# Performance work log

Measured on AMD Instinct MI355X. Metric: run time of the kernel, lower is better.

Reference implementation:

```python
import jax, jax.numpy as jnp
import numpy as np

N_HEADS = 16
NEG_INF = -1e9


def setup_inputs() -> dict:
    key = jax.random.key(0)
    ks = jax.random.split(key, 6)
    B, S, D = 2, 2048, 1024
    scale = 0.02
    return {
        "x": jax.random.normal(ks[0], (B, S, D), dtype=jnp.float32),
        "padding_mask": jnp.ones((B, S), dtype=jnp.float32),
        "wq_w": jax.random.normal(ks[1], (D, D), dtype=jnp.float32) * scale,
        "wq_b": jnp.zeros((D,), dtype=jnp.float32),
        "wk_w": jax.random.normal(ks[2], (D, D), dtype=jnp.float32) * scale,
        "wk_b": jnp.zeros((D,), dtype=jnp.float32),
        "wv_w": jax.random.normal(ks[3], (D, D), dtype=jnp.float32) * scale,
        "wv_b": jnp.zeros((D,), dtype=jnp.float32),
        "wo_w": jax.random.normal(ks[4], (D, D), dtype=jnp.float32) * scale,
        "wo_b": jnp.zeros((D,), dtype=jnp.float32),
    }


def _split_heads(t, B, S, H, depth):
    # (B, S, D) -> (B, H, S, depth)
    return t.reshape(B, S, H, depth).transpose(0, 2, 1, 3)


def reference(x, padding_mask, wq_w, wq_b, wk_w, wk_b, wv_w, wv_b, wo_w, wo_b):
    B, S, D = x.shape
    H = N_HEADS
    depth = D // H

    q = _split_heads(x @ wq_w + wq_b, B, S, H, depth)
    k = _split_heads(x @ wk_w + wk_b, B, S, H, depth)
    v = _split_heads(x @ wv_w + wv_b, B, S, H, depth)

    scale = jnp.sqrt(jnp.asarray(depth, dtype=jnp.float32))
    logits = jnp.einsum('bhqd,bhkd->bhqk', q, k) / scale  # (B,H,S,S)

    causal = jnp.tril(jnp.ones((S, S), dtype=jnp.float32))  # lower-triangular keep mask
    logits = logits + (1.0 - causal)[None, None] * NEG_INF
    # padding mask: (B, S) -> (B, 1, 1, S), 1 = keep
    logits = logits + (1.0 - padding_mask)[:, None, None, :] * NEG_INF

    attn = jax.nn.softmax(logits, axis=-1)
    # dropout: identity at inference (training=False)
    out = jnp.einsum('bhqk,bhkd->bhqd', attn, v)
    out = out.transpose(0, 2, 1, 3).reshape(B, S, D)
    return out @ wo_w + wo_b
```

## Files before the change

kernel.cpp:

```cpp
#include <hip/hip_runtime.h>
#include <math.h>

#define S_LEN 2048
#define DMODEL 1024
#define NH 16
#define DEPTH 64
#define BATCH 2
#define MTOT (BATCH * S_LEN)

typedef __attribute__((ext_vector_type(8))) short short8;
typedef __attribute__((ext_vector_type(4))) short short4v;
typedef __attribute__((ext_vector_type(4))) float floatx4;

typedef const __attribute__((address_space(1))) unsigned gas_u32;
typedef __attribute__((address_space(3))) unsigned las_u32;

__device__ __forceinline__ short f2bf(float f) {
    union { float f; unsigned u; } v; v.f = f;
    unsigned r = v.u + 0x7fffu + ((v.u >> 16) & 1u);
    return (short)(r >> 16);
}

__device__ __forceinline__ unsigned packbf2(float lo, float hi) {
    union { float f; unsigned u; } a, b;
    a.f = lo; b.f = hi;
    return __builtin_amdgcn_perm(b.u + 0x8000u, a.u + 0x8000u, 0x07060302u);
}

__device__ __forceinline__ floatx4 mfma16(short8 a, short8 b, floatx4 c) {
    return __builtin_amdgcn_mfma_f32_16x16x32_bf16(a, b, c, 0, 0, 0);
}

#if __has_builtin(__builtin_amdgcn_mfma_f32_16x16x16bf16_1k)
__device__ __forceinline__ floatx4 mfma16k16(short4v a, short4v b, floatx4 c) {
    return __builtin_amdgcn_mfma_f32_16x16x16bf16_1k(a, b, c, 0, 0, 0);
}
#else
__device__ __forceinline__ floatx4 mfma16k16(short4v a, short4v b, floatx4 c) {
    asm volatile("v_mfma_f32_16x16x16_bf16 %0, %1, %2, %0\n\ts_nop 7\n\ts_nop 7"
                 : "+v"(c) : "v"(a), "v"(b));
    return c;
}
#endif

__global__ __launch_bounds__(256) void prep_kernel(const float* __restrict__ x,
                                                   short* __restrict__ xb,
                                                   const float* __restrict__ w0, const float* __restrict__ w1,
                                                   const float* __restrict__ w2, const float* __restrict__ w3,
                                                   short* __restrict__ o0, short* __restrict__ o1,
                                                   short* __restrict__ o2, short* __restrict__ o3) {
    const int bid = blockIdx.x;
    const int tid = threadIdx.x;
    if (bid < 4096) {
        int i = (bid * 256 + tid) * 4;
        float4 v = *(const float4*)(x + i);
        short4v o;
        o.x = f2bf(v.x); o.y = f2bf(v.y); o.z = f2bf(v.z); o.w = f2bf(v.w);
        *(short4v*)(xb + i) = o;
        return;
    }
    const int b2 = bid - 4096;
    const int z = b2 >> 10;
    const int rem = b2 & 1023;
    const int bx = rem & 31, by = rem >> 5;
    const float* src; short* dst;
    switch (z) {
        case 0: src = w0; dst = o0; break;
        case 1: src = w1; dst = o1; break;
        case 2: src = w2; dst = o2; break;
        default: src = w3; dst = o3; break;
    }
    __shared__ float tile[32][33];
    const int tx = tid & 31, ty = tid >> 5;
    int c = bx * 32 + tx;
    int r0 = by * 32;
#pragma unroll
    for (int i = 0; i < 4; i++)
        tile[ty + i * 8][tx] = src[(size_t)(r0 + ty + i * 8) * DMODEL + c];
    __syncthreads();
    int co = by * 32 + tx;
    int ro = bx * 32;
#pragma unroll
    for (int i = 0; i < 4; i++)
        dst[(size_t)(ro + ty + i * 8) * DMODEL + co] = f2bf(tile[tx][ty + i * 8]);
}

__device__ __forceinline__ void stage_tile(const short* __restrict__ src, int row0, int k0,
                                           short* dstLds, int tid) {
#pragma unroll
    for (int s = 0; s < 4; s++) {
        const int p = s * 4096 + tid * 16;
        const int q = p ^ (((p >> 7) & 7) << 4);
        const char* srcp = (const char*)src + (size_t)(row0 + (q >> 7)) * (DMODEL * 2)
                         + k0 * 2 + (q & 127);
        __builtin_amdgcn_global_load_lds((gas_u32*)srcp,
                                         (las_u32*)((char*)dstLds + p), 16, 0, 0);
    }
}

__device__ __forceinline__ void gemm_core(const short* __restrict__ A,
                                          const short* __restrict__ Bt,
                                          int m0, int n0,
                                          short* Ab0, short* Ab1, short* Bb0, short* Bb1,
                                          floatx4 acc[4][4]) {
    const int tid = threadIdx.x;
    const int lane = tid & 63;
    const int w = tid >> 6;
    const int wr = w >> 1, wc = w & 1;
    const int l15 = lane & 15, lhi = lane >> 4;
    const int swz = (l15 & 7) << 4;

    stage_tile(A, m0, 0, Ab0, tid);
    stage_tile(Bt, n0, 0, Bb0, tid);
    asm volatile("s_waitcnt vmcnt(0)" ::: "memory");
    __syncthreads();

    for (int ks = 0; ks < 16; ks++) {
        const char* Ac = (const char*)((ks & 1) ? Ab1 : Ab0);
        const char* Bc = (const char*)((ks & 1) ? Bb1 : Bb0);
        if (ks < 15) {
            stage_tile(A, m0, (ks + 1) * 64, (ks & 1) ? Ab0 : Ab1, tid);
            stage_tile(Bt, n0, (ks + 1) * 64, (ks & 1) ? Bb0 : Bb1, tid);
        }
#pragma unroll
        for (int kkb = 0; kkb < 128; kkb += 64) {
            short8 af[4], bf[4];
#pragma unroll
            for (int i = 0; i < 4; i++) {
                int row = wr * 64 + i * 16 + l15;
                af[i] = *(const short8*)(Ac + ((row * 128 + kkb + lhi * 16) ^ swz));
            }
#pragma unroll
            for (int j = 0; j < 4; j++) {
                int row = wc * 64 + j * 16 + l15;
                bf[j] = *(const short8*)(Bc + ((row * 128 + kkb + lhi * 16) ^ swz));
            }
#pragma unroll
            for (int i = 0; i < 4; i++)
#pragma unroll
                for (int j = 0; j < 4; j++)
                    acc[i][j] = mfma16(af[i], bf[j], acc[i][j]);
        }
        asm volatile("s_waitcnt vmcnt(0)" ::: "memory");
        __syncthreads();
    }
}

__global__ __launch_bounds__(256) void gemm_qkv(const short* __restrict__ A,
                                                const short* __restrict__ wq, const short* __restrict__ wk,
                                                const short* __restrict__ wv,
                                                const float* __restrict__ bq, const float* __restrict__ bk,
                                                const float* __restrict__ bv,
                                                short* __restrict__ qh, short* __restrict__ kh,
                                                short* __restrict__ vt) {
    __shared__ __align__(16) short Ab[2][8192];
    __shared__ __align__(16) short Bb[2][8192];
    const int bid = blockIdx.x;
    const int xcd = bid & 7;
    const int slot = bid >> 3;
    const int msub = slot & 3;
    const int c = slot >> 2;
    const int nt = c & 7;
    const int mode = c >> 3;
    const int m0 = (xcd * 4 + msub) * 128;
    const int n0 = nt * 128;

    const short* Bt = (mode == 0) ? wq : (mode == 1) ? wk : wv;
    const float* bias = (mode == 0) ? bq : (mode == 1) ? bk : bv;

    floatx4 acc[4][4];
    floatx4 z = {0.f, 0.f, 0.f, 0.f};
#pragma unroll
    for (int i = 0; i < 4; i++)
#pragma unroll
        for (int j = 0; j < 4; j++) acc[i][j] = z;

    gemm_core(A, Bt, m0, n0, Ab[0], Ab[1], Bb[0], Bb[1], acc);

    const int lane = threadIdx.x & 63;
    const int w = threadIdx.x >> 6;
    const int wr = w >> 1, wc = w & 1;
    const int l15 = lane & 15, lhi = lane >> 4;
    const float qscale = (mode == 0) ? 0.125f : 1.0f;
#pragma unroll
    for (int i = 0; i < 4; i++) {
#pragma unroll
        for (int j = 0; j < 4; j++) {
            int n = n0 + wc * 64 + j * 16 + l15;
            float bv_ = bias[n];
            int h = n >> 6, d = n & 63;
            int mbase = m0 + wr * 64 + i * 16 + (lhi << 2);
#pragma unroll
            for (int r = 0; r < 4; r++) {
                int m = mbase + r;
                int b = m >> 11, s = m & 2047;
                short val = f2bf((acc[i][j][r] + bv_) * qscale);
                if (mode == 0)
                    qh[((size_t)(b * NH + h) * S_LEN + s) * DEPTH + d] = val;
                else if (mode == 1)
                    kh[((size_t)(b * NH + h) * S_LEN + s) * DEPTH + d] = val;
                else
                    vt[((size_t)(b * NH + h) * DEPTH + d) * S_LEN + s] = val;
            }
        }
    }
}

__global__ __launch_bounds__(256) void gemm_out(const short* __restrict__ A,
                                                const short* __restrict__ Bt,
                                                const float* __restrict__ bias,
                                                float* __restrict__ out) {
    __shared__ __align__(16) short Ab[2][8192];
    __shared__ __align__(16) short Bb[2][8192];
    const int bid = blockIdx.x;
    const int xcd = bid & 7;
    const int slot = bid >> 3;
    const int msub = slot & 3;
    const int nt = slot >> 2;
    const int m0 = (xcd * 4 + msub) * 128;
    const int n0 = nt * 128;

    floatx4 acc[4][4];
    floatx4 z = {0.f, 0.f, 0.f, 0.f};
#pragma unroll
    for (int i = 0; i < 4; i++)
#pragma unroll
        for (int j = 0; j < 4; j++) acc[i][j] = z;

    gemm_core(A, Bt, m0, n0, Ab[0], Ab[1], Bb[0], Bb[1], acc);

    const int lane = threadIdx.x & 63;
    const int w = threadIdx.x >> 6;
    const int wr = w >> 1, wc = w & 1;
    const int l15 = lane & 15, lhi = lane >> 4;
#pragma unroll
    for (int i = 0; i < 4; i++) {
#pragma unroll
        for (int j = 0; j < 4; j++) {
            int n = n0 + wc * 64 + j * 16 + l15;
            float bv_ = bias[n];
            int mbase = m0 + wr * 64 + i * 16 + (lhi << 2);
#pragma unroll
            for (int r = 0; r < 4; r++) {
                int m = mbase + r;
                out[(size_t)m * DMODEL + n] = acc[i][j][r] + bv_;
            }
        }
    }
}

__constant__ int YCHUNK[16] = {15, 13, 11, 9, 7, 5, 3, 1, 0, 2, 4, 6, 8, 10, 12, 14};

__device__ __forceinline__ void stage_kv(const short* __restrict__ kb_j0,
                                         const short* __restrict__ vb, int j0,
                                         short* kt, short* vt_, int wid, int lane) {
#pragma unroll
    for (int s = 0; s < 2; s++) {
        const int seg = (s * 4 + wid) * 1024;
        const int p = seg + lane * 16;
        const int q = p ^ (((p >> 7) & 7) << 4);
        __builtin_amdgcn_global_load_lds((gas_u32*)((const char*)kb_j0 + q),
                                         (las_u32*)((char*)kt + seg), 16, 0, 0);
        const char* vsrc = (const char*)vb + (size_t)(q >> 7) * (S_LEN * 2) + j0 * 2 + (q & 127);
        __builtin_amdgcn_global_load_lds((gas_u32*)vsrc,
                                         (las_u32*)((char*)vt_ + seg), 16, 0, 0);
    }
}

__global__ __launch_bounds__(256, 2) void attn_kernel(const short* __restrict__ qh,
                                                      const short* __restrict__ kh,
                                                      const short* __restrict__ vt,
                                                      const float* __restrict__ pm,
                                                      short* __restrict__ ao) {
    __shared__ short kbuf[2][4096];
    __shared__ short vbuf[2][4096];
    const int lane = threadIdx.x & 63;
    const int wid = threadIdx.x >> 6;
    const int bh = blockIdx.x;
    const int chunk = YCHUNK[blockIdx.y];
    const int b = bh >> 4, h = bh & 15;
    const short* qbp = qh + (size_t)bh * S_LEN * DEPTH;
    const short* kb = kh + (size_t)bh * S_LEN * DEPTH;
    const short* vb = vt + (size_t)bh * DEPTH * S_LEN;
    const float* pmb = pm + b * S_LEN;
    const int l15 = lane & 15, lhi = lane >> 4;
    const int swz = (l15 & 7) << 4;

    const int qwb = chunk * 128 + wid * 32;

    short8 qf[2][2];
#pragma unroll
    for (int qg = 0; qg < 2; qg++)
#pragma unroll
        for (int c = 0; c < 2; c++)
            qf[qg][c] = *(const short8*)(qbp + (size_t)(qwb + qg * 16 + l15) * DEPTH + c * 32 + lhi * 8);

    float m_r[2] = {-1e30f, -1e30f};
    float l_part[2] = {0.f, 0.f};
    floatx4 oacc[2][4];
    floatx4 z = {0.f, 0.f, 0.f, 0.f};
#pragma unroll
    for (int qg = 0; qg < 2; qg++)
#pragma unroll
        for (int dt = 0; dt < 4; dt++) oacc[qg][dt] = z;

    const int NT = 2 * chunk + 2;
    stage_kv(kb, vb, 0, kbuf[0], vbuf[0], wid, lane);
    __syncthreads();

    for (int t = 0; t < NT; t++) {
        const int cur = t & 1;
        if (t + 1 < NT)
            stage_kv(kb + (size_t)(t + 1) * 64 * DEPTH, vb, (t + 1) * 64,
                     kbuf[cur ^ 1], vbuf[cur ^ 1], wid, lane);
        const int j0 = t * 64;
        if (j0 <= qwb + 31) {
            const short* kt = kbuf[cur];
            const short* vtile = vbuf[cur];
            short8 kf[4][2];
#pragma unroll
            for (int tt = 0; tt < 4; tt++)
#pragma unroll
                for (int c = 0; c < 2; c++) {
                    int off = (((tt * 16 + l15) * 128) + c * 64 + lhi * 16) ^ swz;
                    kf[tt][c] = *(const short8*)((const char*)kt + off);
                }
            floatx4 sacc[2][4];
#pragma unroll
            for (int qg = 0; qg < 2; qg++)
#pragma unroll
                for (int tt = 0; tt < 4; tt++) sacc[qg][tt] = z;
#pragma unroll
            for (int tt = 0; tt < 4; tt++)
#pragma unroll
                for (int c = 0; c < 2; c++) {
                    sacc[0][tt] = mfma16(kf[tt][c], qf[0][c], sacc[0][tt]);
                    sacc[1][tt] = mfma16(kf[tt][c], qf[1][c], sacc[1][tt]);
                }
            short4v vf[4][4];
#pragma unroll
            for (int tt = 0; tt < 4; tt++)
#pragma unroll
                for (int dt = 0; dt < 4; dt++) {
                    int off = (((dt * 16 + l15) * 128) + tt * 32 + lhi * 8) ^ swz;
                    vf[tt][dt] = *(const short4v*)((const char*)vtile + off);
                }
            float pd[16];
#pragma unroll
            for (int tt = 0; tt < 4; tt++) {
                float4 pmv = *(const float4*)(pmb + j0 + tt * 16 + lhi * 4);
                pd[tt * 4 + 0] = (1.f - pmv.x) * -1e9f;
                pd[tt * 4 + 1] = (1.f - pmv.y) * -1e9f;
                pd[tt * 4 + 2] = (1.f - pmv.z) * -1e9f;
                pd[tt * 4 + 3] = (1.f - pmv.w) * -1e9f;
            }
#pragma unroll
            for (int qg = 0; qg < 2; qg++) {
                const int q = qwb + qg * 16 + l15;
                const bool domask = (j0 + 63 > qwb + qg * 16);
                float mx = -1e30f;
#pragma unroll
                for (int tt = 0; tt < 4; tt++)
#pragma unroll
                    for (int r = 0; r < 4; r++) {
                        float v = sacc[qg][tt][r] + pd[tt * 4 + r];
                        if (domask) {
                            int key = j0 + tt * 16 + lhi * 4 + r;
                            v = (key > q) ? -1e30f : v;
                        }
                        sacc[qg][tt][r] = v;
                        mx = fmaxf(mx, v);
                    }
                if (!__all(mx <= m_r[qg] + 12.0f)) {
                    mx = fmaxf(mx, __shfl_xor(mx, 16, 64));
                    mx = fmaxf(mx, __shfl_xor(mx, 32, 64));
                    float mnew = fmaxf(m_r[qg], mx);
                    float sf = __expf(m_r[qg] - mnew);
                    m_r[qg] = mnew;
                    l_part[qg] *= sf;
#pragma unroll
                    for (int r = 0; r < 4; r++) {
                        float sfr = __shfl(sf, lhi * 4 + r, 64);
#pragma unroll
                        for (int dt = 0; dt < 4; dt++) oacc[qg][dt][r] *= sfr;
                    }
                }
#pragma unroll
                for (int tt = 0; tt < 4; tt++) {
                    float p0 = __expf(sacc[qg][tt][0] - m_r[qg]);
                    float p1 = __expf(sacc[qg][tt][1] - m_r[qg]);
                    float p2 = __expf(sacc[qg][tt][2] - m_r[qg]);
                    float p3 = __expf(sacc[qg][tt][3] - m_r[qg]);
                    l_part[qg] += (p0 + p1) + (p2 + p3);
                    union { unsigned u[2]; short4v s; } cv;
                    cv.u[0] = packbf2(p0, p1);
                    cv.u[1] = packbf2(p2, p3);
#pragma unroll
                    for (int dt = 0; dt < 4; dt++)
                        oacc[qg][dt] = mfma16k16(cv.s, vf[tt][dt], oacc[qg][dt]);
                }
            }
        }
        asm volatile("s_waitcnt vmcnt(0)" ::: "memory");
        __syncthreads();
    }

#pragma unroll
    for (int qg = 0; qg < 2; qg++) {
        float lsum = l_part[qg];
        lsum += __shfl_xor(lsum, 16, 64);
        lsum += __shfl_xor(lsum, 32, 64);
        float rinv[4];
#pragma unroll
        for (int r = 0; r < 4; r++)
            rinv[r] = 1.0f / __shfl(lsum, lhi * 4 + r, 64);
#pragma unroll
        for (int dt = 0; dt < 4; dt++) {
            int d = dt * 16 + l15;
#pragma unroll
            for (int r = 0; r < 4; r++) {
                int row = qwb + qg * 16 + lhi * 4 + r;
                float o = oacc[qg][dt][r] * rinv[r];
                ao[((size_t)(b * S_LEN) + row) * DMODEL + h * DEPTH + d] = f2bf(o);
            }
        }
    }
}

extern "C" void kernel_launch(void* const* d_in, const int* in_sizes, int n_in,
                              void* d_out, int out_size, void* d_ws, size_t ws_size,
                              hipStream_t stream) {
    const float* x    = (const float*)d_in[0];
    const float* pm   = (const float*)d_in[1];
    const float* wq_w = (const float*)d_in[2];
    const float* wq_b = (const float*)d_in[3];
    const float* wk_w = (const float*)d_in[4];
    const float* wk_b = (const float*)d_in[5];
    const float* wv_w = (const float*)d_in[6];
    const float* wv_b = (const float*)d_in[7];
    const float* wo_w = (const float*)d_in[8];
    const float* wo_b = (const float*)d_in[9];
    float* out = (float*)d_out;

    char* ws = (char*)d_ws;
    const size_t MB = 1024 * 1024;
    short* xb  = (short*)(ws);
    short* wqb = (short*)(ws + 8 * MB);
    short* wkb = (short*)(ws + 10 * MB);
    short* wvb = (short*)(ws + 12 * MB);
    short* wob = (short*)(ws + 14 * MB);
    short* qh  = (short*)(ws + 16 * MB);
    short* kh  = (short*)(ws + 24 * MB);
    short* vt  = (short*)(ws + 32 * MB);
    short* ao  = (short*)(ws + 40 * MB);

    prep_kernel<<<8192, 256, 0, stream>>>(x, xb, wq_w, wk_w, wv_w, wo_w,
                                          wqb, wkb, wvb, wob);
    gemm_qkv<<<768, 256, 0, stream>>>(xb, wqb, wkb, wvb, wq_b, wk_b, wv_b,
                                      qh, kh, vt);
    attn_kernel<<<dim3(32, 16), 256, 0, stream>>>(qh, kh, vt, pm, ao);
    gemm_out<<<256, 256, 0, stream>>>(ao, wob, wo_b, out);
}
```

Baseline: 129.8 us.

## Use triple-buffered 32-wide K stages with partial vmcnt waits in GEMM core

```diff
diff --git a/kernel.cpp b/kernel.cpp
--- a/kernel.cpp
+++ b/kernel.cpp
@@ -85,14 +85,14 @@
         dst[(size_t)(ro + ty + i * 8) * DMODEL + co] = f2bf(tile[tx][ty + i * 8]);
 }
 
-__device__ __forceinline__ void stage_tile(const short* __restrict__ src, int row0, int k0,
-                                           short* dstLds, int tid) {
-#pragma unroll
-    for (int s = 0; s < 4; s++) {
+__device__ __forceinline__ void stage32(const short* __restrict__ src, int row0, int k0,
+                                        short* dstLds, int tid) {
+#pragma unroll
+    for (int s = 0; s < 2; s++) {
         const int p = s * 4096 + tid * 16;
-        const int q = p ^ (((p >> 7) & 7) << 4);
-        const char* srcp = (const char*)src + (size_t)(row0 + (q >> 7)) * (DMODEL * 2)
-                         + k0 * 2 + (q & 127);
+        const int q = p ^ (((p >> 7) & 3) << 4);
+        const char* srcp = (const char*)src + (size_t)(row0 + (q >> 6)) * (DMODEL * 2)
+                         + k0 * 2 + (q & 63);
         __builtin_amdgcn_global_load_lds((gas_u32*)srcp,
                                          (las_u32*)((char*)dstLds + p), 16, 0, 0);
     }
@@ -101,48 +101,51 @@
 __device__ __forceinline__ void gemm_core(const short* __restrict__ A,
                                           const short* __restrict__ Bt,
                                           int m0, int n0,
-                                          short* Ab0, short* Ab1, short* Bb0, short* Bb1,
+                                          short* Ab, short* Bb,
                                           floatx4 acc[4][4]) {
     const int tid = threadIdx.x;
     const int lane = tid & 63;
     const int w = tid >> 6;
     const int wr = w >> 1, wc = w & 1;
     const int l15 = lane & 15, lhi = lane >> 4;
-    const int swz = (l15 & 7) << 4;
-
-    stage_tile(A, m0, 0, Ab0, tid);
-    stage_tile(Bt, n0, 0, Bb0, tid);
-    asm volatile("s_waitcnt vmcnt(0)" ::: "memory");
-    __syncthreads();
-
-    for (int ks = 0; ks < 16; ks++) {
-        const char* Ac = (const char*)((ks & 1) ? Ab1 : Ab0);
-        const char* Bc = (const char*)((ks & 1) ? Bb1 : Bb0);
-        if (ks < 15) {
-            stage_tile(A, m0, (ks + 1) * 64, (ks & 1) ? Ab0 : Ab1, tid);
-            stage_tile(Bt, n0, (ks + 1) * 64, (ks & 1) ? Bb0 : Bb1, tid);
-        }
-#pragma unroll
-        for (int kkb = 0; kkb < 128; kkb += 64) {
-            short8 af[4], bf[4];
-#pragma unroll
-            for (int i = 0; i < 4; i++) {
-                int row = wr * 64 + i * 16 + l15;
-                af[i] = *(const short8*)(Ac + ((row * 128 + kkb + lhi * 16) ^ swz));
-            }
-#pragma unroll
-            for (int j = 0; j < 4; j++) {
-                int row = wc * 64 + j * 16 + l15;
-                bf[j] = *(const short8*)(Bc + ((row * 128 + kkb + lhi * 16) ^ swz));
-            }
-#pragma unroll
-            for (int i = 0; i < 4; i++)
-#pragma unroll
-                for (int j = 0; j < 4; j++)
-                    acc[i][j] = mfma16(af[i], bf[j], acc[i][j]);
-        }
-        asm volatile("s_waitcnt vmcnt(0)" ::: "memory");
-        __syncthreads();
+
+    int aoff[4], boff[4];
+#pragma unroll
+    for (int i = 0; i < 4; i++) {
+        int arow = wr * 64 + i * 16 + l15;
+        aoff[i] = (arow * 64 + lhi * 16) ^ (((arow >> 1) & 3) << 4);
+        int brow = wc * 64 + i * 16 + l15;
+        boff[i] = (brow * 64 + lhi * 16) ^ (((brow >> 1) & 3) << 4);
+    }
+
+    stage32(A, m0, 0, Ab, tid);
+    stage32(Bt, n0, 0, Bb, tid);
+    stage32(A, m0, 32, Ab + 4096, tid);
+    stage32(Bt, n0, 32, Bb + 4096, tid);
+
+    for (int ks = 0; ks < 32; ks++) {
+        if (ks < 30) {
+            asm volatile("s_waitcnt vmcnt(4)" ::: "memory");
+        } else {
+            asm volatile("s_waitcnt vmcnt(0)" ::: "memory");
+        }
+        asm volatile("s_barrier" ::: "memory");
+        if (ks + 2 < 32) {
+            stage32(A, m0, (ks + 2) * 32, Ab + ((ks + 2) % 3) * 4096, tid);
+            stage32(Bt, n0, (ks + 2) * 32, Bb + ((ks + 2) % 3) * 4096, tid);
+        }
+        const char* Ac = (const char*)(Ab + (ks % 3) * 4096);
+        const char* Bc = (const char*)(Bb + (ks % 3) * 4096);
+        short8 af[4], bf[4];
+#pragma unroll
+        for (int i = 0; i < 4; i++) af[i] = *(const short8*)(Ac + aoff[i]);
+#pragma unroll
+        for (int j = 0; j < 4; j++) bf[j] = *(const short8*)(Bc + boff[j]);
+#pragma unroll
+        for (int i = 0; i < 4; i++)
+#pragma unroll
+            for (int j = 0; j < 4; j++)
+                acc[i][j] = mfma16(af[i], bf[j], acc[i][j]);
     }
 }
 
@@ -153,8 +156,8 @@
                                                 const float* __restrict__ bv,
                                                 short* __restrict__ qh, short* __restrict__ kh,
                                                 short* __restrict__ vt) {
-    __shared__ __align__(16) short Ab[2][8192];
-    __shared__ __align__(16) short Bb[2][8192];
+    __shared__ __align__(16) short Ab[3 * 4096];
+    __shared__ __align__(16) short Bb[3 * 4096];
     const int bid = blockIdx.x;
     const int xcd = bid & 7;
     const int slot = bid >> 3;
@@ -175,7 +178,7 @@
 #pragma unroll
         for (int j = 0; j < 4; j++) acc[i][j] = z;
 
-    gemm_core(A, Bt, m0, n0, Ab[0], Ab[1], Bb[0], Bb[1], acc);
+    gemm_core(A, Bt, m0, n0, Ab, Bb, acc);
 
     const int lane = threadIdx.x & 63;
     const int w = threadIdx.x >> 6;
@@ -210,8 +213,8 @@
                                                 const short* __restrict__ Bt,
                                                 const float* __restrict__ bias,
                                                 float* __restrict__ out) {
-    __shared__ __align__(16) short Ab[2][8192];
-    __shared__ __align__(16) short Bb[2][8192];
+    __shared__ __align__(16) short Ab[3 * 4096];
+    __shared__ __align__(16) short Bb[3 * 4096];
     const int bid = blockIdx.x;
     const int xcd = bid & 7;
     const int slot = bid >> 3;
@@ -227,7 +230,7 @@
 #pragma unroll
         for (int j = 0; j < 4; j++) acc[i][j] = z;
 
-    gemm_core(A, Bt, m0, n0, Ab[0], Ab[1], Bb[0], Bb[1], acc);
+    gemm_core(A, Bt, m0, n0, Ab, Bb, acc);
 
     const int lane = threadIdx.x & 63;
     const int w = threadIdx.x >> 6;
```

Measured after the change: 148.8 us. 14.7% more time.

## Load GEMM B operand directly into registers, drop B LDS staging, add MFMA priority

Applied to the files above, without the earlier changes.

```diff
diff --git a/kernel.cpp b/kernel.cpp
--- a/kernel.cpp
+++ b/kernel.cpp
@@ -98,10 +98,33 @@
     }
 }
 
+__device__ __forceinline__ void loadB(const short* __restrict__ bbase, int ks, short8 bf[8]) {
+#pragma unroll
+    for (int j = 0; j < 4; j++)
+#pragma unroll
+        for (int kk = 0; kk < 2; kk++)
+            bf[j * 2 + kk] = *(const short8*)(bbase + (size_t)(j * 16) * DMODEL + ks * 64 + kk * 32);
+}
+
+__device__ __forceinline__ void mfma_step(const char* Ac, const int aoffs[4][2],
+                                          const short8 bf[8], floatx4 acc[4][4]) {
+#pragma unroll
+    for (int kk = 0; kk < 2; kk++) {
+        short8 af[4];
+#pragma unroll
+        for (int i = 0; i < 4; i++) af[i] = *(const short8*)(Ac + aoffs[i][kk]);
+#pragma unroll
+        for (int i = 0; i < 4; i++)
+#pragma unroll
+            for (int j = 0; j < 4; j++)
+                acc[i][j] = mfma16(af[i], bf[j * 2 + kk], acc[i][j]);
+    }
+}
+
 __device__ __forceinline__ void gemm_core(const short* __restrict__ A,
                                           const short* __restrict__ Bt,
                                           int m0, int n0,
-                                          short* Ab0, short* Ab1, short* Bb0, short* Bb1,
+                                          short* Ab0, short* Ab1,
                                           floatx4 acc[4][4]) {
     const int tid = threadIdx.x;
     const int lane = tid & 63;
@@ -110,51 +133,48 @@
     const int l15 = lane & 15, lhi = lane >> 4;
     const int swz = (l15 & 7) << 4;
 
+    int aoffs[4][2];
+#pragma unroll
+    for (int i = 0; i < 4; i++) {
+        int row = wr * 64 + i * 16 + l15;
+#pragma unroll
+        for (int kk = 0; kk < 2; kk++)
+            aoffs[i][kk] = ((row * 128) + kk * 64 + lhi * 16) ^ swz;
+    }
+    const short* bbase = Bt + (size_t)(n0 + wc * 64 + l15) * DMODEL + lhi * 8;
+
+    short8 b0[8], b1[8];
     stage_tile(A, m0, 0, Ab0, tid);
-    stage_tile(Bt, n0, 0, Bb0, tid);
+    loadB(bbase, 0, b0);
     asm volatile("s_waitcnt vmcnt(0)" ::: "memory");
     __syncthreads();
 
-    for (int ks = 0; ks < 16; ks++) {
-        const char* Ac = (const char*)((ks & 1) ? Ab1 : Ab0);
-        const char* Bc = (const char*)((ks & 1) ? Bb1 : Bb0);
-        if (ks < 15) {
-            stage_tile(A, m0, (ks + 1) * 64, (ks & 1) ? Ab0 : Ab1, tid);
-            stage_tile(Bt, n0, (ks + 1) * 64, (ks & 1) ? Bb0 : Bb1, tid);
-        }
-#pragma unroll
-        for (int kkb = 0; kkb < 128; kkb += 64) {
-            short8 af[4], bf[4];
-#pragma unroll
-            for (int i = 0; i < 4; i++) {
-                int row = wr * 64 + i * 16 + l15;
-                af[i] = *(const short8*)(Ac + ((row * 128 + kkb + lhi * 16) ^ swz));
-            }
-#pragma unroll
-            for (int j = 0; j < 4; j++) {
-                int row = wc * 64 + j * 16 + l15;
-                bf[j] = *(const short8*)(Bc + ((row * 128 + kkb + lhi * 16) ^ swz));
-            }
-#pragma unroll
-            for (int i = 0; i < 4; i++)
-#pragma unroll
-                for (int j = 0; j < 4; j++)
-                    acc[i][j] = mfma16(af[i], bf[j], acc[i][j]);
-        }
+    for (int ks = 0; ks < 16; ks += 2) {
+        if (ks + 1 < 16) {
+            stage_tile(A, m0, (ks + 1) * 64, Ab1, tid);
+            loadB(bbase, ks + 1, b1);
+        }
+        mfma_step((const char*)Ab0, aoffs, b0, acc);
         asm volatile("s_waitcnt vmcnt(0)" ::: "memory");
         __syncthreads();
-    }
-}
-
-__global__ __launch_bounds__(256) void gemm_qkv(const short* __restrict__ A,
-                                                const short* __restrict__ wq, const short* __restrict__ wk,
-                                                const short* __restrict__ wv,
-                                                const float* __restrict__ bq, const float* __restrict__ bk,
-                                                const float* __restrict__ bv,
-                                                short* __restrict__ qh, short* __restrict__ kh,
-                                                short* __restrict__ vt) {
+        if (ks + 2 < 16) {
+            stage_tile(A, m0, (ks + 2) * 64, Ab0, tid);
+            loadB(bbase, ks + 2, b0);
+        }
+        mfma_step((const char*)Ab1, aoffs, b1, acc);
+        asm volatile("s_waitcnt vmcnt(0)" ::: "memory");
+        __syncthreads();
+    }
+}
+
+__global__ __launch_bounds__(256, 3) void gemm_qkv(const short* __restrict__ A,
+                                                   const short* __restrict__ wq, const short* __restrict__ wk,
+                                                   const short* __restrict__ wv,
+                                                   const float* __restrict__ bq, const float* __restrict__ bk,
+                                                   const float* __restrict__ bv,
+                                                   short* __restrict__ qh, short* __restrict__ kh,
+                                                   short* __restrict__ vt) {
     __shared__ __align__(16) short Ab[2][8192];
-    __shared__ __align__(16) short Bb[2][8192];
     const int bid = blockIdx.x;
     const int xcd = bid & 7;
     const int slot = bid >> 3;
@@ -175,7 +195,7 @@
 #pragma unroll
         for (int j = 0; j < 4; j++) acc[i][j] = z;
 
-    gemm_core(A, Bt, m0, n0, Ab[0], Ab[1], Bb[0], Bb[1], acc);
+    gemm_core(A, Bt, m0, n0, Ab[0], Ab[1], acc);
 
     const int lane = threadIdx.x & 63;
     const int w = threadIdx.x >> 6;
@@ -206,12 +226,11 @@
     }
 }
 
-__global__ __launch_bounds__(256) void gemm_out(const short* __restrict__ A,
-                                                const short* __restrict__ Bt,
-                                                const float* __restrict__ bias,
-                                                float* __restrict__ out) {
+__global__ __launch_bounds__(256, 3) void gemm_out(const short* __restrict__ A,
+                                                   const short* __restrict__ Bt,
+                                                   const float* __restrict__ bias,
+                                                   float* __restrict__ out) {
     __shared__ __align__(16) short Ab[2][8192];
-    __shared__ __align__(16) short Bb[2][8192];
     const int bid = blockIdx.x;
     const int xcd = bid & 7;
     const int slot = bid >> 3;
@@ -227,7 +246,7 @@
 #pragma unroll
         for (int j = 0; j < 4; j++) acc[i][j] = z;
 
-    gemm_core(A, Bt, m0, n0, Ab[0], Ab[1], Bb[0], Bb[1], acc);
+    gemm_core(A, Bt, m0, n0, Ab[0], Ab[1], acc);
 
     const int lane = threadIdx.x & 63;
     const int w = threadIdx.x >> 6;
@@ -330,6 +349,7 @@
             for (int qg = 0; qg < 2; qg++)
 #pragma unroll
                 for (int tt = 0; tt < 4; tt++) sacc[qg][tt] = z;
+            __builtin_amdgcn_s_setprio(1);
 #pragma unroll
             for (int tt = 0; tt < 4; tt++)
 #pragma unroll
@@ -337,6 +357,7 @@
                     sacc[0][tt] = mfma16(kf[tt][c], qf[0][c], sacc[0][tt]);
                     sacc[1][tt] = mfma16(kf[tt][c], qf[1][c], sacc[1][tt]);
                 }
+            __builtin_amdgcn_s_setprio(0);
             short4v vf[4][4];
 #pragma unroll
             for (int tt = 0; tt < 4; tt++)
@@ -395,9 +416,11 @@
                     union { unsigned u[2]; short4v s; } cv;
                     cv.u[0] = packbf2(p0, p1);
                     cv.u[1] = packbf2(p2, p3);
+                    __builtin_amdgcn_s_setprio(1);
 #pragma unroll
                     for (int dt = 0; dt < 4; dt++)
                         oacc[qg][dt] = mfma16k16(cv.s, vf[tt][dt], oacc[qg][dt]);
+                    __builtin_amdgcn_s_setprio(0);
                 }
             }
         }
```

After: 187.5 us. 44.5% more time.
